# Performance work log

Hardware: AMD Instinct MI355X
Metric: run time of the kernel (lower is better)

Reference implementation:

```python
import jax, jax.numpy as jnp
import numpy as np
from jax import lax

EPS = 1e-5
DIM_1D, DIM_2D, CH, L, B = 788, 210, 64, 384, 1
DILATIONS = (1, 2, 4, 2, 1)


def inorm(x, gamma, beta, axes):
    # InstanceNorm: normalize over spatial axes per (batch, channel), affine params per channel
    mu = jnp.mean(x, axis=axes, keepdims=True)
    var = jnp.mean(jnp.square(x - mu), axis=axes, keepdims=True)
    xn = (x - mu) * lax.rsqrt(var + EPS)
    shape = [1] * x.ndim
    shape[1] = x.shape[1]
    return xn * gamma.reshape(shape) + beta.reshape(shape)


def inorm_noaffine(x, axes):
    mu = jnp.mean(x, axis=axes, keepdims=True)
    var = jnp.mean(jnp.square(x - mu), axis=axes, keepdims=True)
    return (x - mu) * lax.rsqrt(var + EPS)


def conv3x3(x, w, b, d):
    y = lax.conv_general_dilated(x, w, window_strides=(1, 1),
                                 padding=[(d, d), (d, d)], rhs_dilation=(d, d),
                                 dimension_numbers=('NCHW', 'OIHW', 'NCHW'))
    return y + b.reshape(1, -1, 1, 1)


def setup_inputs() -> dict:
    key = jax.random.key(0)
    ks = jax.random.split(key, 16)
    s = 0.02
    inp = {
        'x_1d': jax.random.normal(ks[0], (B, DIM_1D, L), jnp.float32),
        'x_2d': jax.random.normal(ks[1], (B, DIM_2D, L, L), jnp.float32),
        'W1': jax.random.normal(ks[2], (CH, 2 * DIM_1D), jnp.float32) * s,
        'g1': jnp.ones((CH,), jnp.float32), 'b1': jnp.zeros((CH,), jnp.float32),
        'W2': jax.random.normal(ks[3], (CH, DIM_2D), jnp.float32) * s,
        'g2': jnp.ones((CH,), jnp.float32), 'b2': jnp.zeros((CH,), jnp.float32),
        'W3': jax.random.normal(ks[4], (CH, 2 * CH), jnp.float32) * s,
        'g3': jnp.ones((CH,), jnp.float32), 'b3': jnp.zeros((CH,), jnp.float32),
        'res_w': jax.random.normal(ks[5], (5, 2, CH, CH, 3, 3), jnp.float32) * s,
        'res_b': jnp.zeros((5, 2, CH), jnp.float32),
        'res_g': jnp.ones((5, 2, CH), jnp.float32),
        'res_beta': jnp.zeros((5, 2, CH), jnp.float32),
    }
    return inp


def reference(x_1d, x_2d, W1, g1, b1, W2, g2, b2, W3, g3, b3,
              res_w, res_b, res_g, res_beta):
    # pre-norms (no affine)
    x1 = inorm_noaffine(x_1d, axes=(2,))            # [B, D1, L]
    x2 = inorm_noaffine(x_2d, axes=(2, 3))          # [B, D2, L, L]

    # pair_conv1: 1x1 conv on concat(row-expand, col-expand) of x1.
    # Mathematically: W1a @ x1 broadcast over j  +  W1b @ x1 broadcast over i.
    W1a, W1b = W1[:, :DIM_1D], W1[:, DIM_1D:]
    row = jnp.einsum('cd,bdl->bcl', W1a, x1)        # [B, C, L] (row term, index i)
    col = jnp.einsum('cd,bdl->bcl', W1b, x1)        # [B, C, L] (col term, index j)
    pair1 = row[:, :, :, None] + col[:, :, None, :]  # [B, C, L, L]
    pair1 = jax.nn.leaky_relu(inorm(pair1, g1, b1, axes=(2, 3)), 0.01)

    # pair_conv2: 1x1 conv on x2
    pair2 = jnp.einsum('cd,bdij->bcij', W2, x2)
    pair2 = jax.nn.leaky_relu(inorm(pair2, g2, b2, axes=(2, 3)), 0.01)

    # pair_conv3: 1x1 conv on concat([pair1, pair2]) -> split weight, sum
    W3a, W3b = W3[:, :CH], W3[:, CH:]
    pair = jnp.einsum('cd,bdij->bcij', W3a, pair1) + jnp.einsum('cd,bdij->bcij', W3b, pair2)
    x = jax.nn.leaky_relu(inorm(pair, g3, b3, axes=(2, 3)), 0.01)

    # ResNet: 5 blocks, each (conv-IN-lrelu) x2 + residual, dropout=0
    for layer in range(5):
        d = DILATIONS[layer]
        res = x
        for k in range(2):
            x = conv3x3(x, res_w[layer, k], res_b[layer, k], d)
            x = jax.nn.leaky_relu(inorm(x, res_g[layer, k], res_beta[layer, k], axes=(2, 3)), 0.01)
        x = x + res
    return x
```

## Files before the change

### kernel.cpp

```cpp
#include <hip/hip_runtime.h>
#include <hip/hip_bf16.h>

typedef __attribute__((ext_vector_type(8)))  short short8;
typedef __attribute__((ext_vector_type(16))) float floatx16;
typedef unsigned short ushort;

constexpr int SL  = 384;
constexpr int N2  = SL * SL;
constexpr int CH  = 64;
constexpr int D1  = 788;
constexpr int D2  = 210;
constexpr int KG2 = 14;
constexpr float EPSF = 1e-5f;

constexpr int TX = 32, TY = 8;
constexpr int NBLK = (SL / TX) * (SL / TY);


__device__ __forceinline__ float lrelu(float v){ return v >= 0.f ? v : 0.01f * v; }
__device__ __forceinline__ ushort f2b(float f){
  __hip_bfloat16 h = __float2bfloat16(f); return *(ushort*)&h;
}
__device__ __forceinline__ float b2f(ushort u){
  __hip_bfloat16 h = *(__hip_bfloat16*)&u; return __bfloat162float(h);
}

__device__ __forceinline__ float wred(float v){
  #pragma unroll
  for (int o = 32; o; o >>= 1) v += __shfl_down(v, o, 64);
  return v;
}

__global__ void stats_k(const float* __restrict__ x, int n, float* __restrict__ part){
  const int c = blockIdx.y, s = blockIdx.x, S = gridDim.x;
  const int chunk = (n + S - 1) / S;
  const int st = s * chunk, en = min(n, st + chunk);
  const float* p = x + (size_t)c * n;
  float sm = 0.f, ss = 0.f;
  for (int i = st + threadIdx.x; i < en; i += blockDim.x){
    float v = p[i]; sm += v; ss += v * v;
  }
  sm = wred(sm); ss = wred(ss);
  __shared__ float aux[8];
  const int wid = threadIdx.x >> 6, lane = threadIdx.x & 63;
  if (lane == 0){ aux[wid] = sm; aux[4 + wid] = ss; }
  __syncthreads();
  if (threadIdx.x == 0){
    part[((size_t)c * S + s) * 2]     = aux[0] + aux[1] + aux[2] + aux[3];
    part[((size_t)c * S + s) * 2 + 1] = aux[4] + aux[5] + aux[6] + aux[7];
  }
}

__global__ void stats_final_k(const float* __restrict__ part, int C, int S, float ninv,
                              float* __restrict__ mean, float* __restrict__ rstd){
  const int c = blockIdx.x * 64 + (threadIdx.x >> 4);
  const int t = threadIdx.x & 15;
  if (c >= C) return;
  float sm = 0.f, ss = 0.f;
  for (int s = t; s < S; s += 16){
    sm += part[((size_t)c * S + s) * 2];
    ss += part[((size_t)c * S + s) * 2 + 1];
  }
  #pragma unroll
  for (int o = 8; o; o >>= 1){ sm += __shfl_down(sm, o, 16); ss += __shfl_down(ss, o, 16); }
  if (t == 0){
    const float m = sm * ninv;
    mean[c] = m;
    rstd[c] = rsqrtf(ss * ninv - m * m + EPSF);
  }
}

__global__ void statsaffine_k(const float* __restrict__ part, int S, float ninv,
                              const float* __restrict__ g, const float* __restrict__ be,
                              int goff, float* __restrict__ ao, float* __restrict__ bo){
  const int c = threadIdx.x >> 4;
  const int t = threadIdx.x & 15;
  float sm = 0.f, ss = 0.f;
  for (int s = t; s < S; s += 16){
    sm += part[((size_t)c * S + s) * 2];
    ss += part[((size_t)c * S + s) * 2 + 1];
  }
  #pragma unroll
  for (int o = 8; o; o >>= 1){ sm += __shfl_down(sm, o, 16); ss += __shfl_down(ss, o, 16); }
  if (t == 0){
    const float m = sm * ninv;
    const float r = rsqrtf(ss * ninv - m * m + EPSF);
    const float a = r * g[goff + c];
    ao[c] = a;
    bo[c] = be[goff + c] - m * a;
  }
}

__global__ void rowcol_k(const float* __restrict__ x1d, const float* __restrict__ W1,
                         const float* __restrict__ r1, float* __restrict__ rcP){
  const int idx = blockIdx.x * 256 + threadIdx.x;
  const int chunk = blockIdx.y;
  const int half = idx / (CH * SL);
  const int rem  = idx % (CH * SL);
  const int c = rem / SL, l = rem % SL;
  const int d0 = chunk * 197, d1 = min(D1, d0 + 197);
  const float* wp = W1 + (size_t)c * (2 * D1) + (size_t)half * D1;
  float acc = 0.f;
  for (int d = d0; d < d1; ++d)
    acc += wp[d] * (x1d[(size_t)d * SL + l] * r1[d]);
  rcP[(size_t)chunk * (2 * CH * SL) + idx] = acc;
}

__global__ void rowcol_stats_k(const float* __restrict__ rcP,
                               float* __restrict__ m1, float* __restrict__ rs1){
  const int c = blockIdx.x;
  float sr = 0, ssr = 0, sc = 0, ssc = 0;
  for (int i = threadIdx.x; i < SL; i += blockDim.x){
    float r = 0, q = 0;
    #pragma unroll
    for (int k = 0; k < 4; ++k){
      r += rcP[(size_t)k * (2*CH*SL) + c * SL + i];
      q += rcP[(size_t)k * (2*CH*SL) + CH*SL + c * SL + i];
    }
    sr += r; ssr += r * r; sc += q; ssc += q * q;
  }
  sr = wred(sr); ssr = wred(ssr); sc = wred(sc); ssc = wred(ssc);
  __shared__ float aux[16];
  const int wid = threadIdx.x >> 6, lane = threadIdx.x & 63;
  if (lane == 0){ aux[wid] = sr; aux[4+wid] = ssr; aux[8+wid] = sc; aux[12+wid] = ssc; }
  __syncthreads();
  if (threadIdx.x == 0){
    float a = 0, b = 0, d = 0, e = 0;
    for (int i = 0; i < 4; ++i){ a += aux[i]; b += aux[4+i]; d += aux[8+i]; e += aux[12+i]; }
    const float mr = a / SL, mc = d / SL;
    const float vr = b / SL - mr * mr, vc = e / SL - mc * mc;
    m1[c]  = mr + mc;
    rs1[c] = rsqrtf(vr + vc + EPSF);
  }
}

__global__ void rowcolT_k(const float* __restrict__ rcP,
                          const float* __restrict__ m1, const float* __restrict__ rs1,
                          const float* __restrict__ g1, const float* __restrict__ b1,
                          float* __restrict__ rowT, float* __restrict__ colT){
  const int i = blockIdx.x * 256 + threadIdx.x;
  const int l = i >> 6, c = i & 63;
  float r = 0, q = 0;
  #pragma unroll
  for (int k = 0; k < 4; ++k){
    r += rcP[(size_t)k * (2*CH*SL) + c * SL + l];
    q += rcP[(size_t)k * (2*CH*SL) + CH*SL + c * SL + l];
  }
  const float a  = rs1[c] * g1[c];
  const float bb = b1[c] - m1[c] * a;
  rowT[i] = r * a + bb;
  colT[i] = q * a;
}

__global__ __launch_bounds__(256) void pair1n_k(const float* __restrict__ rowT,
                                                const float* __restrict__ colT,
                                                ushort* __restrict__ out){
  const size_t q = ((size_t)blockIdx.x * 256 + threadIdx.x) * 16;
  const int R = (int)(q >> 4);
  const int x = R % SL;
  const int t = R / SL;
  const int kc = t & 3, y = t >> 2;
  const int c0 = kc * 16;
  const float4* rp = (const float4*)&rowT[y * 64 + c0];
  const float4* cp = (const float4*)&colT[x * 64 + c0];
  ushort o[16];
  #pragma unroll
  for (int k = 0; k < 4; ++k){
    float4 r = rp[k], cl = cp[k];
    o[4*k]   = f2b(lrelu(r.x + cl.x));
    o[4*k+1] = f2b(lrelu(r.y + cl.y));
    o[4*k+2] = f2b(lrelu(r.z + cl.z));
    o[4*k+3] = f2b(lrelu(r.w + cl.w));
  }
  *(short8*)&out[q]     = *(short8*)&o[0];
  *(short8*)&out[q + 8] = *(short8*)&o[8];
}

__global__ __launch_bounds__(256) void x2cvt_k(const float* __restrict__ x2,
                                               ushort* __restrict__ x2b,
                                               float* __restrict__ part){
  const int g  = blockIdx.y;
  const int p0 = blockIdx.x * 1024;
  const int tid = threadIdx.x;
  float sm[16], ss[16];
  #pragma unroll
  for (int i = 0; i < 16; ++i){ sm[i] = 0.f; ss[i] = 0.f; }
  #pragma unroll
  for (int k = 0; k < 4; ++k){
    const int p = p0 + k * 256 + tid;
    float v[16];
    #pragma unroll
    for (int i = 0; i < 16; ++i){
      const int d = g * 16 + i;
      v[i] = (d < D2) ? x2[(size_t)d * N2 + p] : 0.f;
      sm[i] += v[i]; ss[i] += v[i] * v[i];
    }
    ushort o[16];
    #pragma unroll
    for (int i = 0; i < 16; ++i) o[i] = f2b(v[i]);
    ushort* dp = &x2b[((size_t)g * N2 + p) * 16];
    *(short8*)&dp[0] = *(short8*)&o[0];
    *(short8*)&dp[8] = *(short8*)&o[8];
  }
  __shared__ float aux[4][16][2];
  const int wid = tid >> 6, lane = tid & 63;
  #pragma unroll
  for (int i = 0; i < 16; ++i){
    float a = wred(sm[i]), b = wred(ss[i]);
    if (lane == 0){ aux[wid][i][0] = a; aux[wid][i][1] = b; }
  }
  __syncthreads();
  if (tid < 16){
    const int d = g * 16 + tid;
    if (d < D2){
      float a = aux[0][tid][0] + aux[1][tid][0] + aux[2][tid][0] + aux[3][tid][0];
      float b = aux[0][tid][1] + aux[1][tid][1] + aux[2][tid][1] + aux[3][tid][1];
      part[((size_t)d * gridDim.x + blockIdx.x) * 2]     = a;
      part[((size_t)d * gridDim.x + blockIdx.x) * 2 + 1] = b;
    }
  }
}

__global__ void w2b_k(const float* __restrict__ W2, const float* __restrict__ r2,
                      ushort* __restrict__ w2b){
  const int i = blockIdx.x * 256 + threadIdx.x;
  const int j    = i & 7;
  const int oc   = (i >> 3) & 63;
  const int half = (i >> 9) & 1;
  const int kc   = i >> 10;
  const int d    = kc * 16 + half * 8 + j;
  w2b[i] = (d < D2) ? f2b(W2[(size_t)oc * D2 + d] * r2[d]) : (ushort)0;
}

__global__ __launch_bounds__(256) void pair2m_k(const ushort* __restrict__ x2b,
                                                const ushort* __restrict__ w2b,
                                                ushort* __restrict__ out,
                                                float* __restrict__ part){
  __shared__ __align__(16) unsigned char ldsraw[256 * 144 + 4 * CH * 2 * 4];
  const int tid = threadIdx.x, lane = tid & 63, wid = tid >> 6;
  const int ln = lane & 31, half = lane >> 5;
  const int px0 = blockIdx.x * 256;
  floatx16 acc[2][2];
  #pragma unroll
  for (int mt = 0; mt < 2; ++mt)
    #pragma unroll
    for (int nt = 0; nt < 2; ++nt)
      #pragma unroll
      for (int r = 0; r < 16; ++r) acc[mt][nt][r] = 0.f;

  const int p0w = px0 + wid * 64 + ln;
  #pragma unroll
  for (int kc = 0; kc < KG2; ++kc){
    const ushort* ab = w2b + ((size_t)(kc * 2 + half)) * 512;
    short8 a0 = *(const short8*)&ab[ln * 8];
    short8 a1 = *(const short8*)&ab[256 + ln * 8];
    short8 b0 = *(const short8*)&x2b[((size_t)kc * N2 + p0w) * 16 + half * 8];
    short8 b1 = *(const short8*)&x2b[((size_t)kc * N2 + p0w + 32) * 16 + half * 8];
    acc[0][0] = __builtin_amdgcn_mfma_f32_32x32x16_bf16(a0, b0, acc[0][0], 0, 0, 0);
    acc[1][0] = __builtin_amdgcn_mfma_f32_32x32x16_bf16(a1, b0, acc[1][0], 0, 0, 0);
    acc[0][1] = __builtin_amdgcn_mfma_f32_32x32x16_bf16(a0, b1, acc[0][1], 0, 0, 0);
    acc[1][1] = __builtin_amdgcn_mfma_f32_32x32x16_bf16(a1, b1, acc[1][1], 0, 0, 0);
  }

  ushort* tb = (ushort*)ldsraw;
  float*  sc = (float*)(ldsraw + 256 * 144);
  #pragma unroll
  for (int mt = 0; mt < 2; ++mt)
    #pragma unroll
    for (int nt = 0; nt < 2; ++nt){
      const int pxl = (2*wid + nt) * 32 + ln;
      #pragma unroll
      for (int rq = 0; rq < 4; ++rq){
        const int oc0 = mt*32 + 8*rq + 4*half;
        #pragma unroll
        for (int k = 0; k < 2; ++k){
          const int r = rq*4 + k*2;
          unsigned pk = (unsigned)f2b(acc[mt][nt][r]) | ((unsigned)f2b(acc[mt][nt][r+1]) << 16);
          *(unsigned*)&tb[pxl * 72 + oc0 + k*2] = pk;
        }
      }
    }
  #pragma unroll
  for (int mt = 0; mt < 2; ++mt)
    #pragma unroll
    for (int rq = 0; rq < 4; ++rq)
      #pragma unroll
      for (int t = 0; t < 4; ++t){
        const int r = rq*4 + t;
        float v  = acc[mt][0][r] + acc[mt][1][r];
        float v2 = acc[mt][0][r]*acc[mt][0][r] + acc[mt][1][r]*acc[mt][1][r];
        #pragma unroll
        for (int o = 1; o < 32; o <<= 1){ v += __shfl_xor(v, o, 64); v2 += __shfl_xor(v2, o, 64); }
        if (ln == 0){
          const int oc = mt*32 + 8*rq + 4*half + t;
          sc[(wid*CH + oc)*2] = v; sc[(wid*CH + oc)*2 + 1] = v2;
        }
      }
  __syncthreads();
  {
    const int px = lane & 31, h2 = lane >> 5;
    #pragma unroll
    for (int nt = 0; nt < 2; ++nt){
      const int rr = 2*wid + nt;
      const int p = px0 + rr*32 + px;
      const int y = p / SL, x = p - y * SL;
      #pragma unroll
      for (int h = 0; h < 2; ++h){
        const int kc = h2*2 + h;
        const ushort* sp = &tb[(rr*32 + px) * 72 + kc*16];
        ushort* dp = &out[((size_t)((y*4 + kc) * SL) + x) * 16];
        *(short8*)&dp[0] = *(const short8*)&sp[0];
        *(short8*)&dp[8] = *(const short8*)&sp[8];
      }
    }
  }
  if (tid < CH){
    float sm = 0.f, ss = 0.f;
    #pragma unroll
    for (int w = 0; w < 4; ++w){ sm += sc[(w*CH + tid)*2]; ss += sc[(w*CH + tid)*2 + 1]; }
    part[((size_t)tid * NBLK + blockIdx.x) * 2]     = sm;
    part[((size_t)tid * NBLK + blockIdx.x) * 2 + 1] = ss;
  }
}

__global__ __launch_bounds__(256) void norm_nhwc_k(ushort* __restrict__ x,
                                                   const float* __restrict__ a,
                                                   const float* __restrict__ b){
  const size_t q = ((size_t)blockIdx.x * 256 + threadIdx.x) * 16;
  const int R = (int)(q >> 4);
  const int c0 = ((R / SL) & 3) * 16;
  short8 v0 = *(short8*)&x[q], v1 = *(short8*)&x[q + 8];
  ushort o[16];
  #pragma unroll
  for (int k = 0; k < 8; ++k){
    o[k]   = f2b(lrelu(b2f((ushort)v0[k]) * a[c0+k]   + b[c0+k]));
    o[k+8] = f2b(lrelu(b2f((ushort)v1[k]) * a[c0+8+k] + b[c0+8+k]));
  }
  *(short8*)&x[q]     = *(short8*)&o[0];
  *(short8*)&x[q + 8] = *(short8*)&o[8];
}

__global__ void w3b_k(const float* __restrict__ W3, ushort* __restrict__ w3b){
  const int i = blockIdx.x * 256 + threadIdx.x;
  const int j    = i & 7;
  const int oc   = (i >> 3) & 63;
  const int half = (i >> 9) & 1;
  const int kc   = i >> 10;
  const int e    = kc * 16 + half * 8 + j;
  w3b[i] = f2b(W3[oc * (2 * CH) + e]);
}

__global__ __launch_bounds__(256) void mixm_k(const ushort* __restrict__ A,
                                              const ushort* __restrict__ Bv,
                                              const ushort* __restrict__ w3b,
                                              ushort* __restrict__ out,
                                              float* __restrict__ part){
  __shared__ __align__(16) unsigned char ldsraw[256 * 144 + 4 * CH * 2 * 4];
  const int tid = threadIdx.x, lane = tid & 63, wid = tid >> 6;
  const int ln = lane & 31, half = lane >> 5;
  const int px0 = blockIdx.x * 256;
  floatx16 acc[2][2];
  #pragma unroll
  for (int mt = 0; mt < 2; ++mt)
    #pragma unroll
    for (int nt = 0; nt < 2; ++nt)
      #pragma unroll
      for (int r = 0; r < 16; ++r) acc[mt][nt][r] = 0.f;

  const int p0w = px0 + wid * 64 + ln;
  const int p1w = p0w + 32;
  const int y0 = p0w / SL, x0 = p0w - y0 * SL;
  const int y1 = p1w / SL, x1 = p1w - y1 * SL;
  #pragma unroll
  for (int kc = 0; kc < 8; ++kc){
    const ushort* src = (kc < 4) ? A : Bv;
    const int kcm = kc & 3;
    const ushort* ab = w3b + ((size_t)(kc * 2 + half)) * 512;
    short8 a0 = *(const short8*)&ab[ln * 8];
    short8 a1 = *(const short8*)&ab[256 + ln * 8];
    const size_t r0 = ((size_t)((y0 * 4 + kcm) * SL) + x0) * 16 + half * 8;
    const size_t r1 = ((size_t)((y1 * 4 + kcm) * SL) + x1) * 16 + half * 8;
    short8 b0 = *(const short8*)&src[r0];
    short8 b1 = *(const short8*)&src[r1];
    acc[0][0] = __builtin_amdgcn_mfma_f32_32x32x16_bf16(a0, b0, acc[0][0], 0, 0, 0);
    acc[1][0] = __builtin_amdgcn_mfma_f32_32x32x16_bf16(a1, b0, acc[1][0], 0, 0, 0);
    acc[0][1] = __builtin_amdgcn_mfma_f32_32x32x16_bf16(a0, b1, acc[0][1], 0, 0, 0);
    acc[1][1] = __builtin_amdgcn_mfma_f32_32x32x16_bf16(a1, b1, acc[1][1], 0, 0, 0);
  }

  ushort* tb = (ushort*)ldsraw;
  float*  sc = (float*)(ldsraw + 256 * 144);
  #pragma unroll
  for (int mt = 0; mt < 2; ++mt)
    #pragma unroll
    for (int nt = 0; nt < 2; ++nt){
      const int pxl = (2*wid + nt) * 32 + ln;
      #pragma unroll
      for (int rq = 0; rq < 4; ++rq){
        const int oc0 = mt*32 + 8*rq + 4*half;
        #pragma unroll
        for (int k = 0; k < 2; ++k){
          const int r = rq*4 + k*2;
          unsigned pk = (unsigned)f2b(acc[mt][nt][r]) | ((unsigned)f2b(acc[mt][nt][r+1]) << 16);
          *(unsigned*)&tb[pxl * 72 + oc0 + k*2] = pk;
        }
      }
    }
  #pragma unroll
  for (int mt = 0; mt < 2; ++mt)
    #pragma unroll
    for (int rq = 0; rq < 4; ++rq)
      #pragma unroll
      for (int t = 0; t < 4; ++t){
        const int r = rq*4 + t;
        float v  = acc[mt][0][r] + acc[mt][1][r];
        float v2 = acc[mt][0][r]*acc[mt][0][r] + acc[mt][1][r]*acc[mt][1][r];
        #pragma unroll
        for (int o = 1; o < 32; o <<= 1){ v += __shfl_xor(v, o, 64); v2 += __shfl_xor(v2, o, 64); }
        if (ln == 0){
          const int oc = mt*32 + 8*rq + 4*half + t;
          sc[(wid*CH + oc)*2] = v; sc[(wid*CH + oc)*2 + 1] = v2;
        }
      }
  __syncthreads();
  {
    const int px = lane & 31, h2 = lane >> 5;
    #pragma unroll
    for (int nt = 0; nt < 2; ++nt){
      const int rr = 2*wid + nt;
      const int p = px0 + rr*32 + px;
      const int y = p / SL, x = p - y * SL;
      #pragma unroll
      for (int h = 0; h < 2; ++h){
        const int kc = h2*2 + h;
        const ushort* sp = &tb[(rr*32 + px) * 72 + kc*16];
        ushort* dp = &out[((size_t)((y*4 + kc) * SL) + x) * 16];
        *(short8*)&dp[0] = *(const short8*)&sp[0];
        *(short8*)&dp[8] = *(const short8*)&sp[8];
      }
    }
  }
  if (tid < CH){
    float sm = 0.f, ss = 0.f;
    #pragma unroll
    for (int w = 0; w < 4; ++w){ sm += sc[(w*CH + tid)*2]; ss += sc[(w*CH + tid)*2 + 1]; }
    part[((size_t)tid * NBLK + blockIdx.x) * 2]     = sm;
    part[((size_t)tid * NBLK + blockIdx.x) * 2 + 1] = ss;
  }
}

__global__ __launch_bounds__(256) void norm_res_k(const ushort* __restrict__ src,
                                                  const float* __restrict__ a,
                                                  const float* __restrict__ b,
                                                  float* __restrict__ X,
                                                  ushort* __restrict__ Xb,
                                                  int doRes){
  __shared__ float tf[64 * 68];
  const int tid = threadIdx.x;
  const int p0 = blockIdx.x * 64;
  const int y0 = p0 / SL, x0 = p0 - y0 * SL;
  const int pxl = tid >> 2, kc = tid & 3, c0 = kc * 16;
  {
    const ushort* sp = &src[((size_t)((y0*4 + kc) * SL) + x0 + pxl) * 16];
    short8 v0 = *(const short8*)&sp[0], v1 = *(const short8*)&sp[8];
    #pragma unroll
    for (int k = 0; k < 8; ++k){
      tf[(c0+k)*68 + pxl]   = lrelu(b2f((ushort)v0[k]) * a[c0+k]   + b[c0+k]);
      tf[(c0+8+k)*68 + pxl] = lrelu(b2f((ushort)v1[k]) * a[c0+8+k] + b[c0+8+k]);
    }
  }
  __syncthreads();
  {
    const int c = tid >> 2, part = tid & 3;
    const size_t gb = (size_t)c * N2 + p0 + part * 16;
    float w[16];
    #pragma unroll
    for (int k = 0; k < 16; ++k) w[k] = tf[c*68 + part*16 + k];
    if (doRes){
      #pragma unroll
      for (int k = 0; k < 16; ++k) w[k] += X[gb + k];
      #pragma unroll
      for (int k = 0; k < 16; ++k) tf[c*68 + part*16 + k] = w[k];
    }
    #pragma unroll
    for (int k = 0; k < 16; ++k) X[gb + k] = w[k];
  }
  if (Xb){
    __syncthreads();
    ushort o[16];
    #pragma unroll
    for (int k = 0; k < 16; ++k) o[k] = f2b(tf[(c0+k)*68 + pxl]);
    ushort* xp = &Xb[((size_t)((y0*4 + kc) * SL) + x0 + pxl) * 16];
    *(short8*)&xp[0] = *(short8*)&o[0];
    *(short8*)&xp[8] = *(short8*)&o[8];
  }
}

__global__ void wt_k(const float* __restrict__ w, ushort* __restrict__ wt){
  const int i = blockIdx.x * 256 + threadIdx.x;
  const int j    = i & 7;
  const int oc   = (i >> 3) & 63;
  const int half = (i >> 9) & 1;
  const int kc   = (i >> 10) & 3;
  const int tap  = (i / 4096) % 9;
  const int cv   = i / 36864;
  const int ic   = kc * 16 + half * 8 + j;
  wt[i] = f2b(w[((size_t)(cv * CH + oc) * CH + ic) * 9 + tap]);
}

template<int DIL>
__global__ __launch_bounds__(256, 3) void convd_k(const ushort* __restrict__ in,
                                                  const ushort* __restrict__ wg,
                                                  ushort* __restrict__ out,
                                                  float* __restrict__ part){
  __shared__ __align__(16) unsigned char ldsraw[256 * 144 + 4 * CH * 2 * 4];
  const int tid = threadIdx.x, lane = tid & 63, wid = tid >> 6;
  const int ln = lane & 31, half = lane >> 5;
  const int bx = blockIdx.x % (SL / TX), by = blockIdx.x / (SL / TX);
  const int xg = bx * TX + ln;

  floatx16 acc[2][2];
  #pragma unroll
  for (int mt = 0; mt < 2; ++mt)
    #pragma unroll
    for (int nt = 0; nt < 2; ++nt)
      #pragma unroll
      for (int r = 0; r < 16; ++r) acc[mt][nt][r] = 0.f;

  #pragma unroll
  for (int tap = 0; tap < 9; ++tap){
    const int dy = (tap / 3 - 1) * DIL, dx = (tap % 3 - 1) * DIL;
    const int gx = xg + dx;
    const bool okx = (unsigned)gx < (unsigned)SL;
    const int gy0 = by * TY + 2 * wid + dy;
    const int gy1 = gy0 + 1;
    const bool ok0 = okx && ((unsigned)gy0 < (unsigned)SL);
    const bool ok1 = okx && ((unsigned)gy1 < (unsigned)SL);
    const int rb0 = gy0 * 4 * SL + gx;
    const int rb1 = gy1 * 4 * SL + gx;
    #pragma unroll
    for (int kc = 0; kc < 4; ++kc){
      const ushort* ab = wg + ((size_t)((tap * 4 + kc) * 2 + half)) * 512;
      short8 a0 = *(const short8*)&ab[ln * 8];
      short8 a1 = *(const short8*)&ab[256 + ln * 8];
      const long r0 = (long)(rb0 + kc * SL) * 16 + half * 8;
      const long r1 = (long)(rb1 + kc * SL) * 16 + half * 8;
      short8 b0 = {0,0,0,0,0,0,0,0}, b1 = {0,0,0,0,0,0,0,0};
      if (ok0) b0 = *(const short8*)&in[r0];
      if (ok1) b1 = *(const short8*)&in[r1];
      acc[0][0] = __builtin_amdgcn_mfma_f32_32x32x16_bf16(a0, b0, acc[0][0], 0, 0, 0);
      acc[1][0] = __builtin_amdgcn_mfma_f32_32x32x16_bf16(a1, b0, acc[1][0], 0, 0, 0);
      acc[0][1] = __builtin_amdgcn_mfma_f32_32x32x16_bf16(a0, b1, acc[0][1], 0, 0, 0);
      acc[1][1] = __builtin_amdgcn_mfma_f32_32x32x16_bf16(a1, b1, acc[1][1], 0, 0, 0);
    }
  }

  ushort* tb = (ushort*)ldsraw;
  float*  sc = (float*)(ldsraw + 256 * 144);
  #pragma unroll
  for (int mt = 0; mt < 2; ++mt)
    #pragma unroll
    for (int nt = 0; nt < 2; ++nt){
      const int pxl = (2*wid + nt) * 32 + ln;
      #pragma unroll
      for (int rq = 0; rq < 4; ++rq){
        const int oc0 = mt*32 + 8*rq + 4*half;
        #pragma unroll
        for (int k = 0; k < 2; ++k){
          const int r = rq*4 + k*2;
          unsigned pk = (unsigned)f2b(acc[mt][nt][r]) | ((unsigned)f2b(acc[mt][nt][r+1]) << 16);
          *(unsigned*)&tb[pxl * 72 + oc0 + k*2] = pk;
        }
      }
    }
  #pragma unroll
  for (int mt = 0; mt < 2; ++mt)
    #pragma unroll
    for (int rq = 0; rq < 4; ++rq)
      #pragma unroll
      for (int t = 0; t < 4; ++t){
        const int r = rq*4 + t;
        float v  = acc[mt][0][r] + acc[mt][1][r];
        float v2 = acc[mt][0][r]*acc[mt][0][r] + acc[mt][1][r]*acc[mt][1][r];
        #pragma unroll
        for (int o = 1; o < 32; o <<= 1){ v += __shfl_xor(v, o, 64); v2 += __shfl_xor(v2, o, 64); }
        if (ln == 0){
          const int oc = mt*32 + 8*rq + 4*half + t;
          sc[(wid*CH + oc)*2] = v; sc[(wid*CH + oc)*2 + 1] = v2;
        }
      }
  __syncthreads();
  {
    const int px = lane & 31, h2 = lane >> 5;
    #pragma unroll
    for (int nt = 0; nt < 2; ++nt){
      const int rr = 2*wid + nt;
      const int gy = by*TY + rr;
      #pragma unroll
      for (int h = 0; h < 2; ++h){
        const int kc = h2*2 + h;
        const ushort* sp = &tb[(rr*32 + px) * 72 + kc*16];
        ushort* dp = &out[((size_t)((gy*4 + kc) * SL) + bx*TX + px) * 16];
        *(short8*)&dp[0] = *(const short8*)&sp[0];
        *(short8*)&dp[8] = *(const short8*)&sp[8];
      }
    }
  }
  if (tid < CH){
    float sm = 0.f, ss = 0.f;
    #pragma unroll
    for (int w = 0; w < 4; ++w){ sm += sc[(w*CH + tid)*2]; ss += sc[(w*CH + tid)*2 + 1]; }
    part[((size_t)tid * NBLK + blockIdx.x) * 2]     = sm;
    part[((size_t)tid * NBLK + blockIdx.x) * 2 + 1] = ss;
  }
}

static void launch_conv(int dil, const ushort* src, const ushort* wgl,
                        ushort* dst, float* part, hipStream_t s){
  switch (dil){
    case 1:  convd_k<1><<<NBLK, 256, 0, s>>>(src, wgl, dst, part); break;
    case 2:  convd_k<2><<<NBLK, 256, 0, s>>>(src, wgl, dst, part); break;
    default: convd_k<4><<<NBLK, 256, 0, s>>>(src, wgl, dst, part); break;
  }
}

extern "C" void kernel_launch(void* const* d_in, const int* in_sizes, int n_in,
                              void* d_out, int out_size, void* d_ws, size_t ws_size,
                              hipStream_t stream){
  const float* x1d    = (const float*)d_in[0];
  const float* x2     = (const float*)d_in[1];
  const float* W1     = (const float*)d_in[2];
  const float* g1     = (const float*)d_in[3];
  const float* b1     = (const float*)d_in[4];
  const float* W2     = (const float*)d_in[5];
  const float* res_w  = (const float*)d_in[11];
  const float* res_g  = (const float*)d_in[13];
  const float* res_be = (const float*)d_in[14];
  float* X = (float*)d_out;

  unsigned char* wp = (unsigned char*)d_ws;
  ushort* A   = (ushort*)wp; wp += (size_t)N2 * 64 * 2;
  ushort* Bb  = (ushort*)wp; wp += (size_t)N2 * 64 * 2;
  ushort* Xb  = (ushort*)wp; wp += (size_t)N2 * 64 * 2;
  ushort* x2b = (ushort*)wp; wp += (size_t)KG2 * N2 * 16 * 2;
  ushort* wt  = (ushort*)wp; wp += (size_t)368640 * 2;
  ushort* w3b = (ushort*)wp; wp += (size_t)8192 * 2;
  ushort* w2b = (ushort*)wp; wp += (size_t)14336 * 2;
  float* fw = (float*)wp;
  float* rcP  = fw; fw += 4 * 2 * CH * SL;
  float* rowT = fw; fw += SL * CH;
  float* colT = fw; fw += SL * CH;
  float* s1m  = fw; fw += D1;   float* s1r = fw; fw += D1;
  float* s2m  = fw; fw += 256;  float* s2r = fw; fw += 256;
  float* m1   = fw; fw += 64;   float* rs1 = fw; fw += 64;
  float* aA   = fw; fw += 64;   float* bA  = fw; fw += 64;
  float* aB   = fw; fw += 64;   float* bB  = fw; fw += 64;
  float* part = fw; fw += CH * NBLK * 2;

  stats_k<<<dim3(1, D1), 256, 0, stream>>>(x1d, SL, part);
  stats_final_k<<<13, 1024, 0, stream>>>(part, D1, 1, 1.f / SL, s1m, s1r);
  rowcol_k<<<dim3(2 * CH * SL / 256, 4), 256, 0, stream>>>(x1d, W1, s1r, rcP);
  rowcol_stats_k<<<CH, 256, 0, stream>>>(rcP, m1, rs1);
  rowcolT_k<<<SL * CH / 256, 256, 0, stream>>>(rcP, m1, rs1, g1, b1, rowT, colT);
  pair1n_k<<<N2 * 64 / 4096, 256, 0, stream>>>(rowT, colT, A);

  x2cvt_k<<<dim3(144, KG2), 256, 0, stream>>>(x2, x2b, part);
  stats_final_k<<<4, 1024, 0, stream>>>(part, D2, 144, 1.f / N2, s2m, s2r);
  w2b_k<<<56, 256, 0, stream>>>(W2, s2r, w2b);
  pair2m_k<<<NBLK, 256, 0, stream>>>(x2b, w2b, Bb, part);
  statsaffine_k<<<1, 1024, 0, stream>>>(part, NBLK, 1.f / N2,
      (const float*)d_in[6], (const float*)d_in[7], 0, aA, bA);
  norm_nhwc_k<<<N2 * 64 / 4096, 256, 0, stream>>>(Bb, aA, bA);

  w3b_k<<<32, 256, 0, stream>>>((const float*)d_in[8], w3b);
  mixm_k<<<NBLK, 256, 0, stream>>>(A, Bb, w3b, A, part);
  statsaffine_k<<<1, 1024, 0, stream>>>(part, NBLK, 1.f / N2,
      (const float*)d_in[9], (const float*)d_in[10], 0, aA, bA);
  norm_res_k<<<N2 / 64, 256, 0, stream>>>(A, aA, bA, X, Xb, 0);

  wt_k<<<368640 / 256, 256, 0, stream>>>(res_w, wt);

  const int dil[5] = {1, 2, 4, 2, 1};
  for (int layer = 0; layer < 5; ++layer){
    const int d = dil[layer];
    const int li0 = layer * 2, li1 = li0 + 1;
    launch_conv(d, Xb, wt + (size_t)li0 * 36864, A, part, stream);
    statsaffine_k<<<1, 1024, 0, stream>>>(part, NBLK, 1.f / N2, res_g, res_be, li0 * CH, aA, bA);
    norm_nhwc_k<<<N2 * 64 / 4096, 256, 0, stream>>>(A, aA, bA);
    launch_conv(d, A, wt + (size_t)li1 * 36864, Bb, part, stream);
    statsaffine_k<<<1, 1024, 0, stream>>>(part, NBLK, 1.f / N2, res_g, res_be, li1 * CH, aB, bB);
    norm_res_k<<<N2 / 64, 256, 0, stream>>>(Bb, aB, bB, X,
        (layer == 4) ? nullptr : Xb, 1);
  }
}
```

Before: 1.038 ms.

## Stage conv input halo tiles in LDS and fuse norm into second conv

```diff
diff --git a/kernel.cpp b/kernel.cpp
--- a/kernel.cpp
+++ b/kernel.cpp
@@ -180,27 +180,30 @@
                                                ushort* __restrict__ x2b,
                                                float* __restrict__ part){
   const int g  = blockIdx.y;
-  const int p0 = blockIdx.x * 1024;
+  const int p  = blockIdx.x * 1024 + threadIdx.x * 4;
   const int tid = threadIdx.x;
-  float sm[16], ss[16];
-  #pragma unroll
-  for (int i = 0; i < 16; ++i){ sm[i] = 0.f; ss[i] = 0.f; }
-  #pragma unroll
-  for (int k = 0; k < 4; ++k){
-    const int p = p0 + k * 256 + tid;
-    float v[16];
-    #pragma unroll
-    for (int i = 0; i < 16; ++i){
-      const int d = g * 16 + i;
-      v[i] = (d < D2) ? x2[(size_t)d * N2 + p] : 0.f;
-      sm[i] += v[i]; ss[i] += v[i] * v[i];
-    }
+  float4 v[16];
+  #pragma unroll
+  for (int i = 0; i < 16; ++i){
+    const int d = g * 16 + i;
+    if (d < D2) v[i] = *(const float4*)&x2[(size_t)d * N2 + p];
+    else        v[i] = make_float4(0.f, 0.f, 0.f, 0.f);
+  }
+  #pragma unroll
+  for (int q = 0; q < 4; ++q){
     ushort o[16];
     #pragma unroll
-    for (int i = 0; i < 16; ++i) o[i] = f2b(v[i]);
-    ushort* dp = &x2b[((size_t)g * N2 + p) * 16];
+    for (int i = 0; i < 16; ++i) o[i] = f2b(((const float*)&v[i])[q]);
+    ushort* dp = &x2b[((size_t)g * N2 + p + q) * 16];
     *(short8*)&dp[0] = *(short8*)&o[0];
     *(short8*)&dp[8] = *(short8*)&o[8];
+  }
+  float sm[16], ss[16];
+  #pragma unroll
+  for (int i = 0; i < 16; ++i){
+    const float* vp = (const float*)&v[i];
+    sm[i] = vp[0] + vp[1] + vp[2] + vp[3];
+    ss[i] = vp[0]*vp[0] + vp[1]*vp[1] + vp[2]*vp[2] + vp[3]*vp[3];
   }
   __shared__ float aux[4][16][2];
   const int wid = tid >> 6, lane = tid & 63;
@@ -508,16 +511,25 @@
   wt[i] = f2b(w[((size_t)(cv * CH + oc) * CH + ic) * 9 + tap]);
 }
 
-template<int DIL>
+template<int DIL, bool FUSE>
 __global__ __launch_bounds__(256, 3) void convd_k(const ushort* __restrict__ in,
                                                   const ushort* __restrict__ wg,
+                                                  const float* __restrict__ na,
+                                                  const float* __restrict__ nb,
                                                   ushort* __restrict__ out,
                                                   float* __restrict__ part){
-  __shared__ __align__(16) unsigned char ldsraw[256 * 144 + 4 * CH * 2 * 4];
+  constexpr int TH = TY + 2 * DIL;
+  constexpr int TW = TX + 2 * DIL;
+  constexpr int PHASES = (DIL == 4) ? 2 : 1;
+  constexpr int KCP = 4 / PHASES;
+  constexpr int STAGE_B = KCP * TH * TW * 32;
+  constexpr int EPI_B = 256 * 144 + 4 * CH * 2 * 4;
+  constexpr int LDS_B = STAGE_B > EPI_B ? STAGE_B : EPI_B;
+  __shared__ __align__(16) unsigned char ldsraw[LDS_B];
+
   const int tid = threadIdx.x, lane = tid & 63, wid = tid >> 6;
   const int ln = lane & 31, half = lane >> 5;
   const int bx = blockIdx.x % (SL / TX), by = blockIdx.x / (SL / TX);
-  const int xg = bx * TX + ln;
 
   floatx16 acc[2][2];
   #pragma unroll
@@ -528,33 +540,67 @@
       for (int r = 0; r < 16; ++r) acc[mt][nt][r] = 0.f;
 
   #pragma unroll
-  for (int tap = 0; tap < 9; ++tap){
-    const int dy = (tap / 3 - 1) * DIL, dx = (tap % 3 - 1) * DIL;
-    const int gx = xg + dx;
-    const bool okx = (unsigned)gx < (unsigned)SL;
-    const int gy0 = by * TY + 2 * wid + dy;
-    const int gy1 = gy0 + 1;
-    const bool ok0 = okx && ((unsigned)gy0 < (unsigned)SL);
-    const bool ok1 = okx && ((unsigned)gy1 < (unsigned)SL);
-    const int rb0 = gy0 * 4 * SL + gx;
-    const int rb1 = gy1 * 4 * SL + gx;
-    #pragma unroll
-    for (int kc = 0; kc < 4; ++kc){
-      const ushort* ab = wg + ((size_t)((tap * 4 + kc) * 2 + half)) * 512;
-      short8 a0 = *(const short8*)&ab[ln * 8];
-      short8 a1 = *(const short8*)&ab[256 + ln * 8];
-      const long r0 = (long)(rb0 + kc * SL) * 16 + half * 8;
-      const long r1 = (long)(rb1 + kc * SL) * 16 + half * 8;
-      short8 b0 = {0,0,0,0,0,0,0,0}, b1 = {0,0,0,0,0,0,0,0};
-      if (ok0) b0 = *(const short8*)&in[r0];
-      if (ok1) b1 = *(const short8*)&in[r1];
-      acc[0][0] = __builtin_amdgcn_mfma_f32_32x32x16_bf16(a0, b0, acc[0][0], 0, 0, 0);
-      acc[1][0] = __builtin_amdgcn_mfma_f32_32x32x16_bf16(a1, b0, acc[1][0], 0, 0, 0);
-      acc[0][1] = __builtin_amdgcn_mfma_f32_32x32x16_bf16(a0, b1, acc[0][1], 0, 0, 0);
-      acc[1][1] = __builtin_amdgcn_mfma_f32_32x32x16_bf16(a1, b1, acc[1][1], 0, 0, 0);
-    }
-  }
-
+  for (int ph = 0; ph < PHASES; ++ph){
+    if (ph) __syncthreads();
+    constexpr int PIECES = KCP * TH * TW * 2;
+    for (int t = tid; t < PIECES; t += 256){
+      const int half_ = t & 1;
+      const int idx   = t >> 1;
+      const int rx    = idx % TW;
+      const int rem   = idx / TW;
+      const int ry    = rem % TH;
+      const int kcl   = rem / TH;
+      const int kc    = ph * KCP + kcl;
+      const int gy    = by * TY - DIL + ry;
+      const int gx    = bx * TX - DIL + rx;
+      const unsigned byteoff = ((unsigned)t * 16) ^ (((rx >> 2) & 1) << 4);
+      short8 v = {0,0,0,0,0,0,0,0};
+      if ((unsigned)gy < (unsigned)SL && (unsigned)gx < (unsigned)SL){
+        v = *(const short8*)&in[(((size_t)(gy * 4 + kc)) * SL + gx) * 16 + half_ * 8];
+        if (FUSE){
+          const int c0 = kc * 16 + half_ * 8;
+          float4 a0 = *(const float4*)&na[c0], a1 = *(const float4*)&na[c0 + 4];
+          float4 b0 = *(const float4*)&nb[c0], b1 = *(const float4*)&nb[c0 + 4];
+          ushort o[8];
+          o[0] = f2b(lrelu(b2f((ushort)v[0]) * a0.x + b0.x));
+          o[1] = f2b(lrelu(b2f((ushort)v[1]) * a0.y + b0.y));
+          o[2] = f2b(lrelu(b2f((ushort)v[2]) * a0.z + b0.z));
+          o[3] = f2b(lrelu(b2f((ushort)v[3]) * a0.w + b0.w));
+          o[4] = f2b(lrelu(b2f((ushort)v[4]) * a1.x + b1.x));
+          o[5] = f2b(lrelu(b2f((ushort)v[5]) * a1.y + b1.y));
+          o[6] = f2b(lrelu(b2f((ushort)v[6]) * a1.z + b1.z));
+          o[7] = f2b(lrelu(b2f((ushort)v[7]) * a1.w + b1.w));
+          v = *(short8*)o;
+        }
+      }
+      *(short8*)(ldsraw + byteoff) = v;
+    }
+    __syncthreads();
+    #pragma unroll
+    for (int tap = 0; tap < 9; ++tap){
+      const int dy = (tap / 3 - 1) * DIL, dx = (tap % 3 - 1) * DIL;
+      const int ry0 = 2 * wid + dy + DIL;
+      const int rx  = ln + dx + DIL;
+      const unsigned swz = ((unsigned)((rx >> 2) & 1)) << 4;
+      #pragma unroll
+      for (int kcl = 0; kcl < KCP; ++kcl){
+        const int kc = ph * KCP + kcl;
+        const ushort* ab = wg + ((size_t)((tap * 4 + kc) * 2 + half)) * 512;
+        short8 a0 = *(const short8*)&ab[ln * 8];
+        short8 a1 = *(const short8*)&ab[256 + ln * 8];
+        const unsigned bo0 = ((unsigned)((((kcl * TH + ry0) * TW + rx) * 2 + half) * 16)) ^ swz;
+        const unsigned bo1 = ((unsigned)((((kcl * TH + ry0 + 1) * TW + rx) * 2 + half) * 16)) ^ swz;
+        short8 b0 = *(const short8*)(ldsraw + bo0);
+        short8 b1 = *(const short8*)(ldsraw + bo1);
+        acc[0][0] = __builtin_amdgcn_mfma_f32_32x32x16_bf16(a0, b0, acc[0][0], 0, 0, 0);
+        acc[1][0] = __builtin_amdgcn_mfma_f32_32x32x16_bf16(a1, b0, acc[1][0], 0, 0, 0);
+        acc[0][1] = __builtin_amdgcn_mfma_f32_32x32x16_bf16(a0, b1, acc[0][1], 0, 0, 0);
+        acc[1][1] = __builtin_amdgcn_mfma_f32_32x32x16_bf16(a1, b1, acc[1][1], 0, 0, 0);
+      }
+    }
+  }
+
+  __syncthreads();
   ushort* tb = (ushort*)ldsraw;
   float*  sc = (float*)(ldsraw + 256 * 144);
   #pragma unroll
@@ -615,12 +661,21 @@
   }
 }
 
-static void launch_conv(int dil, const ushort* src, const ushort* wgl,
+static void launch_conv(int dil, bool fuse, const ushort* src, const ushort* wgl,
+                        const float* na, const float* nb,
                         ushort* dst, float* part, hipStream_t s){
-  switch (dil){
-    case 1:  convd_k<1><<<NBLK, 256, 0, s>>>(src, wgl, dst, part); break;
-    case 2:  convd_k<2><<<NBLK, 256, 0, s>>>(src, wgl, dst, part); break;
-    default: convd_k<4><<<NBLK, 256, 0, s>>>(src, wgl, dst, part); break;
+  if (fuse){
+    switch (dil){
+      case 1:  convd_k<1,true><<<NBLK, 256, 0, s>>>(src, wgl, na, nb, dst, part); break;
+      case 2:  convd_k<2,true><<<NBLK, 256, 0, s>>>(src, wgl, na, nb, dst, part); break;
+      default: convd_k<4,true><<<NBLK, 256, 0, s>>>(src, wgl, na, nb, dst, part); break;
+    }
+  } else {
+    switch (dil){
+      case 1:  convd_k<1,false><<<NBLK, 256, 0, s>>>(src, wgl, na, nb, dst, part); break;
+      case 2:  convd_k<2,false><<<NBLK, 256, 0, s>>>(src, wgl, na, nb, dst, part); break;
+      default: convd_k<4,false><<<NBLK, 256, 0, s>>>(src, wgl, na, nb, dst, part); break;
+    }
   }
 }
 
@@ -684,10 +739,9 @@
   for (int layer = 0; layer < 5; ++layer){
     const int d = dil[layer];
     const int li0 = layer * 2, li1 = li0 + 1;
-    launch_conv(d, Xb, wt + (size_t)li0 * 36864, A, part, stream);
+    launch_conv(d, false, Xb, wt + (size_t)li0 * 36864, nullptr, nullptr, A, part, stream);
     statsaffine_k<<<1, 1024, 0, stream>>>(part, NBLK, 1.f / N2, res_g, res_be, li0 * CH, aA, bA);
-    norm_nhwc_k<<<N2 * 64 / 4096, 256, 0, stream>>>(A, aA, bA);
-    launch_conv(d, A, wt + (size_t)li1 * 36864, Bb, part, stream);
+    launch_conv(d, true, A, wt + (size_t)li1 * 36864, aA, bA, Bb, part, stream);
     statsaffine_k<<<1, 1024, 0, stream>>>(part, NBLK, 1.f / N2, res_g, res_be, li1 * CH, aB, bB);
     norm_res_k<<<N2 / 64, 256, 0, stream>>>(Bb, aB, bB, X,
         (layer == 4) ? nullptr : Xb, 1);
```

New measurement: 1.040 ms. About the same (+0.2%).
